# Kernel tuning notes

Hardware: AMD Instinct MI355X
Metric: run time of the kernel (lower is better)

## Reference

```python
import jax, jax.numpy as jnp
import numpy as np

N_NODES = 50000
N_EDGES = 800000
NUM_FEATS = 128
HIDDEN = 512
OUT = 2


def setup_inputs() -> dict:
    key = jax.random.key(0)
    k1, k2, k3, k4 = jax.random.split(key, 4)
    X = jax.random.normal(k1, (N_NODES, NUM_FEATS), dtype=jnp.float32)
    edge_index = jax.random.randint(k2, (2, N_EDGES), 0, N_NODES, dtype=jnp.int64)
    W1 = jax.random.normal(k3, (NUM_FEATS, HIDDEN), dtype=jnp.float32) / np.sqrt(NUM_FEATS)
    b1 = jnp.zeros((HIDDEN,), dtype=jnp.float32)
    W2 = jax.random.normal(k4, (HIDDEN, OUT), dtype=jnp.float32) / np.sqrt(HIDDEN)
    b2 = jnp.zeros((OUT,), dtype=jnp.float32)
    return {"X": X, "edge_index": edge_index, "W1": W1, "b1": b1, "W2": W2, "b2": b2}


def _gcn_conv(x, W, b, src, dst, dinv, n):
    # PyG GCNConv: x' = D^{-1/2} (A + I) D^{-1/2} (x W) + b
    xw = x @ W  # [N, C]
    edge_norm = dinv[src] * dinv[dst]  # [E]
    msg = xw[src] * edge_norm[:, None]  # [E, C] gathered messages
    agg = jax.ops.segment_sum(msg, dst, num_segments=n)
    agg = agg + xw * (dinv * dinv)[:, None]  # self-loop contribution
    return agg + b


def reference(X, edge_index, W1, b1, W2, b2):
    n = X.shape[0]
    src, dst = edge_index[0], edge_index[1]
    # degree with self-loops (gcn_norm): deg[i] = in_degree(i) + 1
    deg = jax.ops.segment_sum(jnp.ones_like(dst, dtype=X.dtype), dst, num_segments=n) + 1.0
    dinv = jax.lax.rsqrt(deg)
    h = jax.nn.relu(_gcn_conv(X, W1, b1, src, dst, dinv, n))
    logits = _gcn_conv(h, W2, b2, src, dst, dinv, n)
    # nn.Softmax() on a 2D tensor defaults to dim=1
    return jax.nn.softmax(logits, axis=1)
```

## Files before the change

kernel.cpp:

```cpp
#include <hip/hip_runtime.h>

#define N_FEATS 128
#define HIDDEN 512
#define NPAD 50176
#define ELLW 64
#define NBKT 196
#define SLAB 4608
#define PA_EPB 4096
#define PA_BLOCKS 196
#define XH_BLOCKS 6250
#define GB_HALF 1563

typedef __attribute__((ext_vector_type(4))) float floatx4;
typedef __attribute__((ext_vector_type(8))) short shortx8;
typedef __attribute__((ext_vector_type(8))) unsigned short ushortx8;

__device__ __forceinline__ unsigned short f2bf(float f) {
    union { float f; unsigned u; } a; a.f = f;
    unsigned r = a.u + 0x7fff + ((a.u >> 16) & 1);
    return (unsigned short)(r >> 16);
}

__global__ __launch_bounds__(256) void k_initA(const float* __restrict__ W1,
        unsigned short* __restrict__ w1t, const float* __restrict__ X,
        unsigned short* __restrict__ Xh, const int* __restrict__ src,
        const int* __restrict__ dst, int* __restrict__ bcur,
        unsigned* __restrict__ staging, int E, int N) {
    int b = blockIdx.x, tid = threadIdx.x;
    if (b < PA_BLOCKS) {
        __shared__ int hist[NBKT];
        __shared__ int base[NBKT];
        for (int i = tid; i < NBKT; i += 256) hist[i] = 0;
        __syncthreads();
        #pragma unroll
        for (int i = 0; i < 4; ++i) {
            int e = b * PA_EPB + (i * 256 + tid) * 4;
            if (e + 3 < E) {
                int4 d4 = *reinterpret_cast<const int4*>(dst + e);
                atomicAdd(&hist[d4.x >> 8], 1);
                atomicAdd(&hist[d4.y >> 8], 1);
                atomicAdd(&hist[d4.z >> 8], 1);
                atomicAdd(&hist[d4.w >> 8], 1);
            } else {
                for (int k = 0; k < 4; ++k)
                    if (e + k < E) atomicAdd(&hist[dst[e + k] >> 8], 1);
            }
        }
        __syncthreads();
        for (int i = tid; i < NBKT; i += 256) {
            int c = hist[i];
            base[i] = c ? atomicAdd(&bcur[i], c) : 0;
            hist[i] = 0;
        }
        __syncthreads();
        #pragma unroll
        for (int i = 0; i < 4; ++i) {
            int e = b * PA_EPB + (i * 256 + tid) * 4;
            if (e + 3 < E) {
                int4 d4 = *reinterpret_cast<const int4*>(dst + e);
                int4 s4 = *reinterpret_cast<const int4*>(src + e);
                #define PUT(dd, ss) { int bk = (dd) >> 8; int r = atomicAdd(&hist[bk], 1); \
                    int pos = base[bk] + r; if (pos < SLAB) \
                    staging[(size_t)bk * SLAB + pos] = ((unsigned)(ss) << 8) | (unsigned)((dd) & 255); }
                PUT(d4.x, s4.x) PUT(d4.y, s4.y) PUT(d4.z, s4.z) PUT(d4.w, s4.w)
            } else {
                for (int k = 0; k < 4; ++k)
                    if (e + k < E) { int dd = dst[e + k], ss = src[e + k]; PUT(dd, ss) }
                #undef PUT
            }
        }
    } else if (b < PA_BLOCKS + 16) {
        __shared__ unsigned short t[64][65];
        int bb = b - PA_BLOCKS;
        int ki = bb >> 3, ni = bb & 7;
        #pragma unroll
        for (int i = 0; i < 16; ++i) {
            int idx = tid + i * 256;
            int r = idx >> 6, c = idx & 63;
            t[r][c] = f2bf(W1[(ki * 64 + r) * 512 + ni * 64 + c]);
        }
        __syncthreads();
        #pragma unroll
        for (int i = 0; i < 16; ++i) {
            int idx = tid + i * 256;
            int rn = idx >> 6, ck = idx & 63;
            w1t[(ni * 64 + rn) * 128 + ki * 64 + ck] = t[ck][rn];
        }
    } else {
        int idx = (b - PA_BLOCKS - 16) * 256 + tid;
        if (idx < N * 32) {
            float4 v = reinterpret_cast<const float4*>(X)[idx];
            ushort4 o;
            o.x = f2bf(v.x); o.y = f2bf(v.y); o.z = f2bf(v.z); o.w = f2bf(v.w);
            reinterpret_cast<ushort4*>(Xh)[idx] = o;
        }
    }
}

__global__ __launch_bounds__(256) void k_bucketB(const int* __restrict__ bcur,
        const unsigned* __restrict__ staging, int* __restrict__ ell,
        int* __restrict__ cursor, float* __restrict__ dinvs) {
    __shared__ int cur[256];
    int b = blockIdx.x, tid = threadIdx.x;
    cur[tid] = 0;
    __syncthreads();
    int cnt = bcur[b];
    if (cnt > SLAB) cnt = SLAB;
    for (int j = tid; j < cnt; j += 256) {
        unsigned v = staging[(size_t)b * SLAB + j];
        int dl = (int)(v & 255u);
        int s = (int)(v >> 8);
        int pos = atomicAdd(&cur[dl], 1);
        if (pos < ELLW) ell[(size_t)((b << 8) + dl) * ELLW + pos] = s;
    }
    __syncthreads();
    int c = cur[tid];
    cursor[(b << 8) + tid] = c;
    dinvs[(b << 8) + tid] = rsqrtf((float)c + 1.0f);
}

__global__ __launch_bounds__(256) void k_gather(const int* __restrict__ cursor,
        const float* __restrict__ dinvs, const int* __restrict__ ell,
        const unsigned short* __restrict__ Xh, unsigned short* __restrict__ aggAh, int N) {
    int b = blockIdx.x;
    int half = (b >= GB_HALF) ? 1 : 0;
    int t = (b - half * GB_HALF) * 256 + threadIdx.x;
    int node = t >> 3;
    int lane = t & 7;
    if (node >= N) return;
    int cnt = cursor[node];
    float dv = dinvs[node];
    int lim = cnt < ELLW ? cnt : ELLW;
    int coff = half * 8 + lane;
    const ushortx8* Xv = reinterpret_cast<const ushortx8*>(Xh);
    #define BF(x) ({ union { unsigned u; float f; } _c; _c.u = (unsigned)(x) << 16; _c.f; })
    union U8 { ushortx8 v; unsigned short s[8]; };
    U8 sv; sv.v = Xv[(size_t)node * 16 + coff];
    float a[8];
    #pragma unroll
    for (int k = 0; k < 8; ++k) a[k] = dv * BF(sv.s[k]);
    const int* row = ell + (size_t)node * ELLW;
    int j = 0;
    int4 nxt;
    if (lim >= 4) nxt = *reinterpret_cast<const int4*>(row);
    for (; j + 4 <= lim; j += 4) {
        int4 s4 = nxt;
        if (j + 8 <= lim) nxt = *reinterpret_cast<const int4*>(row + j + 4);
        float w0 = dinvs[s4.x], w1 = dinvs[s4.y], w2 = dinvs[s4.z], w3 = dinvs[s4.w];
        U8 u0, u1, u2, u3;
        u0.v = Xv[(size_t)s4.x * 16 + coff];
        u1.v = Xv[(size_t)s4.y * 16 + coff];
        u2.v = Xv[(size_t)s4.z * 16 + coff];
        u3.v = Xv[(size_t)s4.w * 16 + coff];
        #pragma unroll
        for (int k = 0; k < 8; ++k)
            a[k] += w0 * BF(u0.s[k]) + w1 * BF(u1.s[k]) + w2 * BF(u2.s[k]) + w3 * BF(u3.s[k]);
    }
    for (; j < lim; ++j) {
        int s = row[j];
        float w = dinvs[s];
        U8 u; u.v = Xv[(size_t)s * 16 + coff];
        #pragma unroll
        for (int k = 0; k < 8; ++k) a[k] += w * BF(u.s[k]);
    }
    #undef BF
    union { ushortx8 v; unsigned short s[8]; } o;
    #pragma unroll
    for (int k = 0; k < 8; ++k) o.s[k] = f2bf(a[k] * dv);
    reinterpret_cast<ushortx8*>(aggAh)[(size_t)node * 16 + coff] = o.v;
}

__global__ __launch_bounds__(256) void k_fused_mfma(
        const unsigned short* __restrict__ aggAh, const unsigned short* __restrict__ w1t,
        const float* __restrict__ b1, const float* __restrict__ W2,
        const float* __restrict__ dinvs, float2* __restrict__ lps, int N) {
    __shared__ unsigned short As[128][136];
    __shared__ unsigned short Bs[128][136];
    __shared__ float b1s[HIDDEN];
    __shared__ float W2s[HIDDEN * 2];

    const int tid = threadIdx.x;
    const int wave = tid >> 6;
    const int lane = tid & 63;
    const int quad = lane >> 4;
    const int l16 = lane & 15;
    const int m0 = blockIdx.x * 128;

    for (int i = tid; i < HIDDEN; i += 256) b1s[i] = b1[i];
    for (int i = tid; i < HIDDEN * 2; i += 256) W2s[i] = W2[i];

    #pragma unroll
    for (int it = 0; it < 8; ++it) {
        int flat = (tid + it * 256) * 8;
        int r = flat >> 7, c = flat & 127;
        int gm = m0 + r;
        shortx8 v = {0, 0, 0, 0, 0, 0, 0, 0};
        if (gm < N) v = *reinterpret_cast<const shortx8*>(aggAh + (size_t)gm * 128 + c);
        *reinterpret_cast<shortx8*>(&As[r][c]) = v;
    }

    float accL0[2][4], accL1[2][4];
    #pragma unroll
    for (int s = 0; s < 2; ++s)
        #pragma unroll
        for (int r = 0; r < 4; ++r) { accL0[s][r] = 0.f; accL1[s][r] = 0.f; }

    for (int n0 = 0; n0 < HIDDEN; n0 += 128) {
        #pragma unroll
        for (int it = 0; it < 8; ++it) {
            int flat = (tid + it * 256) * 8;
            int r = flat >> 7, c = flat & 127;
            *reinterpret_cast<shortx8*>(&Bs[r][c]) =
                *reinterpret_cast<const shortx8*>(w1t + (size_t)(n0 + r) * 128 + c);
        }
        __syncthreads();

        floatx4 acc[2][8];
        #pragma unroll
        for (int s = 0; s < 2; ++s)
            #pragma unroll
            for (int nt = 0; nt < 8; ++nt) acc[s][nt] = (floatx4){0.f, 0.f, 0.f, 0.f};

        #pragma unroll
        for (int ks = 0; ks < 4; ++ks) {
            shortx8 af0 = *reinterpret_cast<const shortx8*>(&As[wave * 32 + l16][ks * 32 + quad * 8]);
            shortx8 af1 = *reinterpret_cast<const shortx8*>(&As[wave * 32 + 16 + l16][ks * 32 + quad * 8]);
            #pragma unroll
            for (int nt = 0; nt < 8; ++nt) {
                shortx8 bf = *reinterpret_cast<const shortx8*>(&Bs[nt * 16 + l16][ks * 32 + quad * 8]);
                acc[0][nt] = __builtin_amdgcn_mfma_f32_16x16x32_bf16(af0, bf, acc[0][nt], 0, 0, 0);
                acc[1][nt] = __builtin_amdgcn_mfma_f32_16x16x32_bf16(af1, bf, acc[1][nt], 0, 0, 0);
            }
        }

        #pragma unroll
        for (int nt = 0; nt < 8; ++nt) {
            int col = n0 + nt * 16 + l16;
            float bb = b1s[col];
            float w20 = W2s[col * 2 + 0];
            float w21 = W2s[col * 2 + 1];
            #pragma unroll
            for (int s = 0; s < 2; ++s) {
                #pragma unroll
                for (int r = 0; r < 4; ++r) {
                    float h = acc[s][nt][r] + bb;
                    h = h > 0.f ? h : 0.f;
                    accL0[s][r] += h * w20;
                    accL1[s][r] += h * w21;
                }
            }
        }
        __syncthreads();
    }

    #pragma unroll
    for (int off = 1; off < 16; off <<= 1) {
        #pragma unroll
        for (int s = 0; s < 2; ++s)
            #pragma unroll
            for (int r = 0; r < 4; ++r) {
                accL0[s][r] += __shfl_xor(accL0[s][r], off);
                accL1[s][r] += __shfl_xor(accL1[s][r], off);
            }
    }
    if (l16 == 0) {
        #pragma unroll
        for (int s = 0; s < 2; ++s)
            #pragma unroll
            for (int r = 0; r < 4; ++r) {
                int gm = m0 + wave * 32 + s * 16 + quad * 4 + r;
                if (gm < N) {
                    float dv = dinvs[gm];
                    lps[gm] = make_float2(dv * accL0[s][r], dv * accL1[s][r]);
                }
            }
    }
}

__global__ __launch_bounds__(256) void k_final(const int* __restrict__ cursor,
        const float* __restrict__ dinvs, const int* __restrict__ ell,
        const float2* __restrict__ lps, const float* __restrict__ b2,
        float* __restrict__ out, int N) {
    int t = blockIdx.x * 256 + threadIdx.x;
    int node = t >> 3;
    int lane = t & 7;
    if (node >= N) return;
    int cnt = cursor[node];
    int lim = cnt < ELLW ? cnt : ELLW;
    const int* row = ell + (size_t)node * ELLW;
    float a0 = 0.f, a1 = 0.f;
    for (int j = lane; j < lim; j += 8) {
        float2 v = lps[row[j]];
        a0 += v.x;
        a1 += v.y;
    }
    #pragma unroll
    for (int off = 1; off < 8; off <<= 1) {
        a0 += __shfl_xor(a0, off);
        a1 += __shfl_xor(a1, off);
    }
    if (lane == 0) {
        float dv = dinvs[node];
        float2 self = lps[node];
        float l0 = dv * (a0 + self.x) + b2[0];
        float l1 = dv * (a1 + self.y) + b2[1];
        float m = fmaxf(l0, l1);
        float e0 = __expf(l0 - m), e1 = __expf(l1 - m);
        float inv = 1.0f / (e0 + e1);
        out[(size_t)node * 2 + 0] = e0 * inv;
        out[(size_t)node * 2 + 1] = e1 * inv;
    }
}

extern "C" void kernel_launch(void* const* d_in, const int* in_sizes, int n_in,
                              void* d_out, int out_size, void* d_ws, size_t ws_size,
                              hipStream_t stream) {
    const float* X  = (const float*)d_in[0];
    const int* ei   = (const int*)d_in[1];
    const float* W1 = (const float*)d_in[2];
    const float* b1 = (const float*)d_in[3];
    const float* W2 = (const float*)d_in[4];
    const float* b2 = (const float*)d_in[5];
    float* out = (float*)d_out;

    const int N = in_sizes[0] / N_FEATS;
    const int E = in_sizes[1] / 2;
    const int* src = ei;
    const int* dst = ei + E;

    int* cursor = (int*)d_ws;
    int* bcur   = cursor + NPAD;
    int* ell    = bcur + 256;
    float2* lps = (float2*)(ell + (size_t)NPAD * ELLW);
    float* dinvs = (float*)(lps + NPAD);
    unsigned short* w1t = (unsigned short*)(dinvs + NPAD);
    unsigned short* Xh  = w1t + 512 * 128;
    unsigned* staging = (unsigned*)(Xh + (size_t)NPAD * 128);
    unsigned short* aggAh = (unsigned short*)staging;

    hipMemsetAsync(bcur, 0, 256 * sizeof(int), stream);
    k_initA   <<<PA_BLOCKS + 16 + XH_BLOCKS, 256, 0, stream>>>(
                  W1, w1t, X, Xh, src, dst, bcur, staging, E, N);
    k_bucketB <<<NBKT, 256, 0, stream>>>(bcur, staging, ell, cursor, dinvs);
    k_gather  <<<2 * GB_HALF, 256, 0, stream>>>(cursor, dinvs, ell, Xh, aggAh, N);
    k_fused_mfma<<<(N + 127) / 128, 256, 0, stream>>>(aggAh, w1t, b1, W2, dinvs, lps, N);
    k_final   <<<((size_t)N * 8 + 255) / 256, 256, 0, stream>>>(cursor, dinvs, ell, lps, b2, out, N);
}
```

Measured before the change: 165.7 us.

## Fuse neighbor gather into MFMA GEMM and replace ELL with bucketed CSR

The separate gather kernel is merged into the fused MFMA kernel. Each 512-thread block now aggregates its 128 rows straight into shared memory, so the aggregated bf16 matrix no longer makes a round trip through global memory. The fixed-width ELL adjacency becomes a compact per-bucket CSR built with a shared-memory prefix scan, which cuts index memory and drops the degree-64 truncation. The cost is fewer, larger blocks doing irregular gather work ahead of the GEMM, so the gather and MFMA phases cannot overlap across kernels.

```diff
diff --git a/kernel.cpp b/kernel.cpp
--- a/kernel.cpp
+++ b/kernel.cpp
@@ -3,13 +3,11 @@
 #define N_FEATS 128
 #define HIDDEN 512
 #define NPAD 50176
-#define ELLW 64
 #define NBKT 196
 #define SLAB 4608
 #define PA_EPB 4096
 #define PA_BLOCKS 196
 #define XH_BLOCKS 6250
-#define GB_HALF 1563
 
 typedef __attribute__((ext_vector_type(4))) float floatx4;
 typedef __attribute__((ext_vector_type(8))) short shortx8;
@@ -20,6 +18,7 @@
     unsigned r = a.u + 0x7fff + ((a.u >> 16) & 1);
     return (unsigned short)(r >> 16);
 }
+#define BF(x) ({ union { unsigned u; float f; } _c; _c.u = (unsigned)(x) << 16; _c.f; })
 
 __global__ __launch_bounds__(256) void k_initA(const float* __restrict__ W1,
         unsigned short* __restrict__ w1t, const float* __restrict__ X,
@@ -98,138 +97,151 @@
 }
 
 __global__ __launch_bounds__(256) void k_bucketB(const int* __restrict__ bcur,
-        const unsigned* __restrict__ staging, int* __restrict__ ell,
-        int* __restrict__ cursor, float* __restrict__ dinvs) {
-    __shared__ int cur[256];
+        const unsigned* __restrict__ staging, int* __restrict__ csr_g,
+        int* __restrict__ offs_g, int* __restrict__ cursor, float* __restrict__ dinvs) {
+    __shared__ int hist[256];
+    __shared__ int offs_l[256];
+    __shared__ int sc[256];
     int b = blockIdx.x, tid = threadIdx.x;
-    cur[tid] = 0;
+    hist[tid] = 0;
     __syncthreads();
     int cnt = bcur[b];
     if (cnt > SLAB) cnt = SLAB;
+    const unsigned* st = staging + (size_t)b * SLAB;
+    for (int j = tid; j < cnt; j += 256) atomicAdd(&hist[st[j] & 255u], 1);
+    __syncthreads();
+    int c = hist[tid];
+    sc[tid] = c;
+    __syncthreads();
+    #pragma unroll
+    for (int off = 1; off < 256; off <<= 1) {
+        int t = (tid >= off) ? sc[tid - off] : 0;
+        __syncthreads();
+        sc[tid] += t;
+        __syncthreads();
+    }
+    int excl = sc[tid] - c;
+    offs_l[tid] = excl;
+    int node = (b << 8) + tid;
+    cursor[node] = c;
+    dinvs[node] = rsqrtf((float)c + 1.0f);
+    offs_g[node] = b * SLAB + excl;
+    hist[tid] = 0;
+    __syncthreads();
     for (int j = tid; j < cnt; j += 256) {
-        unsigned v = staging[(size_t)b * SLAB + j];
+        unsigned v = st[j];
         int dl = (int)(v & 255u);
         int s = (int)(v >> 8);
-        int pos = atomicAdd(&cur[dl], 1);
-        if (pos < ELLW) ell[(size_t)((b << 8) + dl) * ELLW + pos] = s;
-    }
-    __syncthreads();
-    int c = cur[tid];
-    cursor[(b << 8) + tid] = c;
-    dinvs[(b << 8) + tid] = rsqrtf((float)c + 1.0f);
-}
-
-__global__ __launch_bounds__(256) void k_gather(const int* __restrict__ cursor,
-        const float* __restrict__ dinvs, const int* __restrict__ ell,
-        const unsigned short* __restrict__ Xh, unsigned short* __restrict__ aggAh, int N) {
-    int b = blockIdx.x;
-    int half = (b >= GB_HALF) ? 1 : 0;
-    int t = (b - half * GB_HALF) * 256 + threadIdx.x;
-    int node = t >> 3;
-    int lane = t & 7;
-    if (node >= N) return;
-    int cnt = cursor[node];
-    float dv = dinvs[node];
-    int lim = cnt < ELLW ? cnt : ELLW;
-    int coff = half * 8 + lane;
-    const ushortx8* Xv = reinterpret_cast<const ushortx8*>(Xh);
-    #define BF(x) ({ union { unsigned u; float f; } _c; _c.u = (unsigned)(x) << 16; _c.f; })
-    union U8 { ushortx8 v; unsigned short s[8]; };
-    U8 sv; sv.v = Xv[(size_t)node * 16 + coff];
-    float a[8];
-    #pragma unroll
-    for (int k = 0; k < 8; ++k) a[k] = dv * BF(sv.s[k]);
-    const int* row = ell + (size_t)node * ELLW;
-    int j = 0;
-    int4 nxt;
-    if (lim >= 4) nxt = *reinterpret_cast<const int4*>(row);
-    for (; j + 4 <= lim; j += 4) {
-        int4 s4 = nxt;
-        if (j + 8 <= lim) nxt = *reinterpret_cast<const int4*>(row + j + 4);
-        float w0 = dinvs[s4.x], w1 = dinvs[s4.y], w2 = dinvs[s4.z], w3 = dinvs[s4.w];
-        U8 u0, u1, u2, u3;
-        u0.v = Xv[(size_t)s4.x * 16 + coff];
-        u1.v = Xv[(size_t)s4.y * 16 + coff];
-        u2.v = Xv[(size_t)s4.z * 16 + coff];
-        u3.v = Xv[(size_t)s4.w * 16 + coff];
-        #pragma unroll
-        for (int k = 0; k < 8; ++k)
-            a[k] += w0 * BF(u0.s[k]) + w1 * BF(u1.s[k]) + w2 * BF(u2.s[k]) + w3 * BF(u3.s[k]);
-    }
-    for (; j < lim; ++j) {
-        int s = row[j];
-        float w = dinvs[s];
-        U8 u; u.v = Xv[(size_t)s * 16 + coff];
-        #pragma unroll
-        for (int k = 0; k < 8; ++k) a[k] += w * BF(u.s[k]);
-    }
-    #undef BF
-    union { ushortx8 v; unsigned short s[8]; } o;
-    #pragma unroll
-    for (int k = 0; k < 8; ++k) o.s[k] = f2bf(a[k] * dv);
-    reinterpret_cast<ushortx8*>(aggAh)[(size_t)node * 16 + coff] = o.v;
-}
-
-__global__ __launch_bounds__(256) void k_fused_mfma(
-        const unsigned short* __restrict__ aggAh, const unsigned short* __restrict__ w1t,
+        int p = atomicAdd(&hist[dl], 1);
+        csr_g[b * SLAB + offs_l[dl] + p] = s;
+    }
+}
+
+__global__ __launch_bounds__(512, 4) void k_gather_gemm(
+        const int* __restrict__ cursor, const float* __restrict__ dinvs,
+        const int* __restrict__ offs_g, const int* __restrict__ csr_g,
+        const unsigned short* __restrict__ Xh, const unsigned short* __restrict__ w1t,
         const float* __restrict__ b1, const float* __restrict__ W2,
-        const float* __restrict__ dinvs, float2* __restrict__ lps, int N) {
+        float2* __restrict__ lps, int N) {
     __shared__ unsigned short As[128][136];
     __shared__ unsigned short Bs[128][136];
     __shared__ float b1s[HIDDEN];
     __shared__ float W2s[HIDDEN * 2];
 
     const int tid = threadIdx.x;
+    const int m0 = blockIdx.x * 128;
+    for (int i = tid; i < HIDDEN; i += 512) b1s[i] = b1[i];
+    for (int i = tid; i < HIDDEN * 2; i += 512) W2s[i] = W2[i];
+
+    union U8 { ushortx8 v; unsigned short s[8]; };
+
+    #pragma unroll
+    for (int h = 0; h < 2; ++h) {
+        int r = h * 64 + (tid >> 3);
+        int lane = tid & 7;
+        int gm = m0 + r;
+        if (gm < N) {
+            float dv = dinvs[gm];
+            int beg = offs_g[gm];
+            int cnt = cursor[gm];
+            const ushortx8* Xp = reinterpret_cast<const ushortx8*>(Xh) + ((size_t)gm << 4);
+            U8 sv0, sv1;
+            sv0.v = Xp[lane];
+            sv1.v = Xp[8 + lane];
+            float a0[8], a1[8];
+            #pragma unroll
+            for (int k = 0; k < 8; ++k) { a0[k] = dv * BF(sv0.s[k]); a1[k] = dv * BF(sv1.s[k]); }
+            const int* cp = csr_g + beg;
+            int j = 0;
+            for (; j + 4 <= cnt; j += 4) {
+                int e0 = cp[j], e1 = cp[j + 1], e2 = cp[j + 2], e3 = cp[j + 3];
+                float w0 = dinvs[e0], w1 = dinvs[e1], w2 = dinvs[e2], w3 = dinvs[e3];
+                const ushortx8* x0 = reinterpret_cast<const ushortx8*>(Xh) + ((size_t)e0 << 4);
+                const ushortx8* x1 = reinterpret_cast<const ushortx8*>(Xh) + ((size_t)e1 << 4);
+                const ushortx8* x2 = reinterpret_cast<const ushortx8*>(Xh) + ((size_t)e2 << 4);
+                const ushortx8* x3 = reinterpret_cast<const ushortx8*>(Xh) + ((size_t)e3 << 4);
+                U8 p00, p01, p10, p11, p20, p21, p30, p31;
+                p00.v = x0[lane]; p01.v = x0[8 + lane];
+                p10.v = x1[lane]; p11.v = x1[8 + lane];
+                p20.v = x2[lane]; p21.v = x2[8 + lane];
+                p30.v = x3[lane]; p31.v = x3[8 + lane];
+                #pragma unroll
+                for (int k = 0; k < 8; ++k) {
+                    a0[k] += w0 * BF(p00.s[k]) + w1 * BF(p10.s[k]) + w2 * BF(p20.s[k]) + w3 * BF(p30.s[k]);
+                    a1[k] += w0 * BF(p01.s[k]) + w1 * BF(p11.s[k]) + w2 * BF(p21.s[k]) + w3 * BF(p31.s[k]);
+                }
+            }
+            for (; j < cnt; ++j) {
+                int s = cp[j];
+                float w = dinvs[s];
+                const ushortx8* xp = reinterpret_cast<const ushortx8*>(Xh) + ((size_t)s << 4);
+                U8 q0, q1;
+                q0.v = xp[lane]; q1.v = xp[8 + lane];
+                #pragma unroll
+                for (int k = 0; k < 8; ++k) { a0[k] += w * BF(q0.s[k]); a1[k] += w * BF(q1.s[k]); }
+            }
+            union { shortx8 v; unsigned short s[8]; } o0, o1;
+            #pragma unroll
+            for (int k = 0; k < 8; ++k) { o0.s[k] = f2bf(a0[k] * dv); o1.s[k] = f2bf(a1[k] * dv); }
+            *reinterpret_cast<shortx8*>(&As[r][lane * 8]) = o0.v;
+            *reinterpret_cast<shortx8*>(&As[r][64 + lane * 8]) = o1.v;
+        } else {
+            shortx8 z = {0, 0, 0, 0, 0, 0, 0, 0};
+            *reinterpret_cast<shortx8*>(&As[r][lane * 8]) = z;
+            *reinterpret_cast<shortx8*>(&As[r][64 + lane * 8]) = z;
+        }
+    }
+    __syncthreads();
+
     const int wave = tid >> 6;
-    const int lane = tid & 63;
-    const int quad = lane >> 4;
-    const int l16 = lane & 15;
-    const int m0 = blockIdx.x * 128;
-
-    for (int i = tid; i < HIDDEN; i += 256) b1s[i] = b1[i];
-    for (int i = tid; i < HIDDEN * 2; i += 256) W2s[i] = W2[i];
-
-    #pragma unroll
-    for (int it = 0; it < 8; ++it) {
-        int flat = (tid + it * 256) * 8;
-        int r = flat >> 7, c = flat & 127;
-        int gm = m0 + r;
-        shortx8 v = {0, 0, 0, 0, 0, 0, 0, 0};
-        if (gm < N) v = *reinterpret_cast<const shortx8*>(aggAh + (size_t)gm * 128 + c);
-        *reinterpret_cast<shortx8*>(&As[r][c]) = v;
-    }
-
-    float accL0[2][4], accL1[2][4];
-    #pragma unroll
-    for (int s = 0; s < 2; ++s)
-        #pragma unroll
-        for (int r = 0; r < 4; ++r) { accL0[s][r] = 0.f; accL1[s][r] = 0.f; }
+    const int lane64 = tid & 63;
+    const int quad = lane64 >> 4;
+    const int l16 = lane64 & 15;
+
+    float accL0[4] = {0.f, 0.f, 0.f, 0.f};
+    float accL1[4] = {0.f, 0.f, 0.f, 0.f};
 
     for (int n0 = 0; n0 < HIDDEN; n0 += 128) {
         #pragma unroll
-        for (int it = 0; it < 8; ++it) {
-            int flat = (tid + it * 256) * 8;
+        for (int it = 0; it < 4; ++it) {
+            int flat = (tid + it * 512) * 8;
             int r = flat >> 7, c = flat & 127;
             *reinterpret_cast<shortx8*>(&Bs[r][c]) =
                 *reinterpret_cast<const shortx8*>(w1t + (size_t)(n0 + r) * 128 + c);
         }
         __syncthreads();
 
-        floatx4 acc[2][8];
-        #pragma unroll
-        for (int s = 0; s < 2; ++s)
-            #pragma unroll
-            for (int nt = 0; nt < 8; ++nt) acc[s][nt] = (floatx4){0.f, 0.f, 0.f, 0.f};
+        floatx4 acc[8];
+        #pragma unroll
+        for (int nt = 0; nt < 8; ++nt) acc[nt] = (floatx4){0.f, 0.f, 0.f, 0.f};
 
         #pragma unroll
         for (int ks = 0; ks < 4; ++ks) {
-            shortx8 af0 = *reinterpret_cast<const shortx8*>(&As[wave * 32 + l16][ks * 32 + quad * 8]);
-            shortx8 af1 = *reinterpret_cast<const shortx8*>(&As[wave * 32 + 16 + l16][ks * 32 + quad * 8]);
+            shortx8 af = *reinterpret_cast<const shortx8*>(&As[wave * 16 + l16][ks * 32 + quad * 8]);
             #pragma unroll
             for (int nt = 0; nt < 8; ++nt) {
                 shortx8 bf = *reinterpret_cast<const shortx8*>(&Bs[nt * 16 + l16][ks * 32 + quad * 8]);
-                acc[0][nt] = __builtin_amdgcn_mfma_f32_16x16x32_bf16(af0, bf, acc[0][nt], 0, 0, 0);
-                acc[1][nt] = __builtin_amdgcn_mfma_f32_16x16x32_bf16(af1, bf, acc[1][nt], 0, 0, 0);
+                acc[nt] = __builtin_amdgcn_mfma_f32_16x16x32_bf16(af, bf, acc[nt], 0, 0, 0);
             }
         }
 
@@ -240,14 +252,11 @@
             float w20 = W2s[col * 2 + 0];
             float w21 = W2s[col * 2 + 1];
             #pragma unroll
-            for (int s = 0; s < 2; ++s) {
-                #pragma unroll
-                for (int r = 0; r < 4; ++r) {
-                    float h = acc[s][nt][r] + bb;
-                    h = h > 0.f ? h : 0.f;
-                    accL0[s][r] += h * w20;
-                    accL1[s][r] += h * w21;
-                }
+            for (int r = 0; r < 4; ++r) {
+                float hh = acc[nt][r] + bb;
+                hh = hh > 0.f ? hh : 0.f;
+                accL0[r] += hh * w20;
+                accL1[r] += hh * w21;
             }
         }
         __syncthreads();
@@ -256,41 +265,36 @@
     #pragma unroll
     for (int off = 1; off < 16; off <<= 1) {
         #pragma unroll
-        for (int s = 0; s < 2; ++s)
-            #pragma unroll
-            for (int r = 0; r < 4; ++r) {
-                accL0[s][r] += __shfl_xor(accL0[s][r], off);
-                accL1[s][r] += __shfl_xor(accL1[s][r], off);
-            }
+        for (int r = 0; r < 4; ++r) {
+            accL0[r] += __shfl_xor(accL0[r], off);
+            accL1[r] += __shfl_xor(accL1[r], off);
+        }
     }
     if (l16 == 0) {
         #pragma unroll
-        for (int s = 0; s < 2; ++s)
-            #pragma unroll
-            for (int r = 0; r < 4; ++r) {
-                int gm = m0 + wave * 32 + s * 16 + quad * 4 + r;
-                if (gm < N) {
-                    float dv = dinvs[gm];
-                    lps[gm] = make_float2(dv * accL0[s][r], dv * accL1[s][r]);
-                }
-            }
+        for (int r = 0; r < 4; ++r) {
+            int gm = m0 + wave * 16 + quad * 4 + r;
+            if (gm < N) {
+                float dv = dinvs[gm];
+                lps[gm] = make_float2(dv * accL0[r], dv * accL1[r]);
+            }
+        }
     }
 }
 
 __global__ __launch_bounds__(256) void k_final(const int* __restrict__ cursor,
-        const float* __restrict__ dinvs, const int* __restrict__ ell,
-        const float2* __restrict__ lps, const float* __restrict__ b2,
-        float* __restrict__ out, int N) {
+        const float* __restrict__ dinvs, const int* __restrict__ offs_g,
+        const int* __restrict__ csr_g, const float2* __restrict__ lps,
+        const float* __restrict__ b2, float* __restrict__ out, int N) {
     int t = blockIdx.x * 256 + threadIdx.x;
     int node = t >> 3;
     int lane = t & 7;
     if (node >= N) return;
     int cnt = cursor[node];
-    int lim = cnt < ELLW ? cnt : ELLW;
-    const int* row = ell + (size_t)node * ELLW;
+    int beg = offs_g[node];
     float a0 = 0.f, a1 = 0.f;
-    for (int j = lane; j < lim; j += 8) {
-        float2 v = lps[row[j]];
+    for (int j = lane; j < cnt; j += 8) {
+        float2 v = lps[csr_g[beg + j]];
         a0 += v.x;
         a1 += v.y;
     }
@@ -328,21 +332,22 @@
     const int* src = ei;
     const int* dst = ei + E;
 
-    int* cursor = (int*)d_ws;
-    int* bcur   = cursor + NPAD;
-    int* ell    = bcur + 256;
-    float2* lps = (float2*)(ell + (size_t)NPAD * ELLW);
-    float* dinvs = (float*)(lps + NPAD);
-    unsigned short* w1t = (unsigned short*)(dinvs + NPAD);
+    int* cursor  = (int*)d_ws;
+    int* bcur    = cursor + NPAD;
+    int* offs_g  = bcur + 256;
+    float* dinvs = (float*)(offs_g + NPAD);
+    float2* lps  = (float2*)(dinvs + NPAD);
+    unsigned short* w1t = (unsigned short*)(lps + NPAD);
     unsigned short* Xh  = w1t + 512 * 128;
     unsigned* staging = (unsigned*)(Xh + (size_t)NPAD * 128);
-    unsigned short* aggAh = (unsigned short*)staging;
+    int* csr_g   = (int*)(staging + (size_t)NBKT * SLAB);
 
     hipMemsetAsync(bcur, 0, 256 * sizeof(int), stream);
-    k_initA   <<<PA_BLOCKS + 16 + XH_BLOCKS, 256, 0, stream>>>(
-                  W1, w1t, X, Xh, src, dst, bcur, staging, E, N);
-    k_bucketB <<<NBKT, 256, 0, stream>>>(bcur, staging, ell, cursor, dinvs);
-    k_gather  <<<2 * GB_HALF, 256, 0, stream>>>(cursor, dinvs, ell, Xh, aggAh, N);
-    k_fused_mfma<<<(N + 127) / 128, 256, 0, stream>>>(aggAh, w1t, b1, W2, dinvs, lps, N);
-    k_final   <<<((size_t)N * 8 + 255) / 256, 256, 0, stream>>>(cursor, dinvs, ell, lps, b2, out, N);
-}
+    k_initA      <<<PA_BLOCKS + 16 + XH_BLOCKS, 256, 0, stream>>>(
+                     W1, w1t, X, Xh, src, dst, bcur, staging, E, N);
+    k_bucketB    <<<NBKT, 256, 0, stream>>>(bcur, staging, csr_g, offs_g, cursor, dinvs);
+    k_gather_gemm<<<NPAD / 128, 512, 0, stream>>>(cursor, dinvs, offs_g, csr_g,
+                     Xh, w1t, b1, W2, lps, N);
+    k_final      <<<((size_t)N * 8 + 255) / 256, 256, 0, stream>>>(
+                     cursor, dinvs, offs_g, csr_g, lps, b2, out, N);
+}
```

After: 151.4 us. 1.09x faster.
